# Kernel tuning notes

Hardware: AMD Instinct MI355X
Metric: run time of the kernel (lower is better)

Reference implementation:

```python
import jax, jax.numpy as jnp
import numpy as np

NH, HD, MB = 32, 64, 16        # heads, head_dim, TTT mini-batch size
BASE_LR = 1.0
ROPE_THETA = 10000.0


def _ln(x, w, b, eps):
    mu = x.mean(-1, keepdims=True)
    var = ((x - mu) ** 2).mean(-1, keepdims=True)
    return (x - mu) / jnp.sqrt(var + eps) * w + b


def _rotate_half(x):
    x1, x2 = jnp.split(x, 2, axis=-1)
    return jnp.concatenate([-x2, x1], axis=-1)


def _ln_l2_bwd(x, target, g, b, eps=1e-6):
    # grad of ||LN(x)*g+b - target||^2 / 2 wrt x (fused, as in ttt-lm)
    D = x.shape[-1]
    mu = x.mean(-1, keepdims=True)
    var = ((x - mu) ** 2).mean(-1, keepdims=True)
    std = jnp.sqrt(var + eps)
    xh = (x - mu) / std
    gxh = (g * xh + b - target) * g
    return (D * gxh - gxh.sum(-1, keepdims=True) - xh * (gxh * xh).sum(-1, keepdims=True)) / (D * std)


def _ttt_forward(x, q_w, k_w, v_w, o_w, ttt_lr_w, ttt_lr_b, token_idx_off,
                 ttt_norm_w, ttt_norm_b, W1, b1, post_w, post_b):
    B, L, C = x.shape
    NM = L // MB
    XQ = (x @ q_w).reshape(B, L, NH, HD).transpose(0, 2, 1, 3)  # [B,NH,L,HD]
    XK = (x @ k_w).reshape(B, L, NH, HD).transpose(0, 2, 1, 3)
    XV = (x @ v_w).reshape(B, L, NH, HD).transpose(0, 2, 1, 3)
    # rotary embedding at position_ids % mini_batch_size
    pos = (jnp.arange(L) % MB).astype(jnp.float32)
    inv = 1.0 / (ROPE_THETA ** (jnp.arange(0, HD, 2, dtype=jnp.float32) / HD))
    fr = pos[:, None] * inv[None, :]
    emb = jnp.concatenate([fr, fr], axis=-1)           # [L,HD]
    cos, sin = jnp.cos(emb), jnp.sin(emb)
    XQ = XQ * cos + _rotate_half(XQ) * sin
    XK = XK * cos + _rotate_half(XK) * sin
    # learning-rate gate (eta)
    Xm = x.reshape(B, NM, MB, C)
    ttt_lr = jax.nn.sigmoid(jnp.einsum('bnkc,hdc->bhnkd', Xm, ttt_lr_w)
                            + ttt_lr_b.reshape(1, NH, 1, 1, 1))       # [B,NH,NM,MB,1]
    ttt_lr_eta = BASE_LR * ttt_lr.transpose(0, 1, 2, 4, 3) / HD       # [B,NH,NM,1,MB]
    tok = jnp.maximum(1.0 / jnp.arange(1, MB + 1, dtype=jnp.float32) + token_idx_off, 0.0)
    eta = tok.reshape(1, 1, 1, MB, 1) * ttt_lr_eta                    # [B,NH,NM,MB,MB]

    def tomb(t):  # [B,NH,L,HD] -> [NM,B,NH,MB,HD]
        return t.reshape(B, NH, NM, MB, HD).transpose(2, 0, 1, 3, 4)

    xs = (tomb(XQ), tomb(XK), tomb(XV), eta.transpose(2, 0, 1, 3, 4))
    lw = ttt_norm_w.reshape(1, NH, 1, HD)
    lb = ttt_norm_b.reshape(1, NH, 1, HD)
    tril = jnp.tril(jnp.ones((MB, MB), x.dtype))
    W1s = jnp.broadcast_to(W1, (B, NH, HD, HD)).astype(x.dtype)
    b1s = jnp.broadcast_to(b1, (B, NH, 1, HD)).astype(x.dtype)

    def step(carry, xs_t):
        W1c, b1c = carry
        xq, xk, xv, et = xs_t                      # [B,NH,MB,HD], et [B,NH,MB,MB]
        Z1 = xk @ W1c + b1c
        grad = _ln_l2_bwd(Z1, xv - xk, lw, lb)     # grad of per-head TTT loss wrt Z1
        Attn1 = jnp.tril(xq @ xk.transpose(0, 1, 3, 2))
        b1_bar = b1c - (et * tril) @ grad
        Z1_bar = xq @ W1c - (et * Attn1) @ grad + b1_bar
        last_eta = et[:, :, -1, :, None]           # [B,NH,MB,1]
        W1n = W1c - jnp.einsum('bhki,bhkj->bhij', last_eta * xk, grad)
        b1n = b1c - (last_eta * grad).sum(-2, keepdims=True)
        out = xq + _ln(Z1_bar, lw, lb, 1e-6)
        return (W1n, b1n), out

    _, outs = jax.lax.scan(step, (W1s, b1s), xs)   # outs: [NM,B,NH,MB,HD]
    y = outs.transpose(1, 0, 3, 2, 4).reshape(B, L, C)
    y = _ln(y, post_w, post_b, 1e-6)
    return y @ o_w


def setup_inputs() -> dict:
    key = jax.random.key(0)
    ks = jax.random.split(key, 16)
    B, L, C, DH = 4, 2048, 2048, 1024
    s = 0.02
    return {
        'enc_input': jax.random.normal(ks[0], (B, L, C), jnp.float32),
        'ln1_w': jnp.ones((C,), jnp.float32), 'ln1_b': jnp.zeros((C,), jnp.float32),
        'q_w': jax.random.normal(ks[1], (C, C), jnp.float32) * s,
        'k_w': jax.random.normal(ks[2], (C, C), jnp.float32) * s,
        'v_w': jax.random.normal(ks[3], (C, C), jnp.float32) * s,
        'o_w': jax.random.normal(ks[4], (C, C), jnp.float32) * s,
        'ttt_lr_w': jax.random.normal(ks[5], (NH, 1, C), jnp.float32) * s,
        'ttt_lr_b': jax.random.normal(ks[6], (NH,), jnp.float32) * s,
        'token_idx_off': jax.random.normal(ks[7], (MB,), jnp.float32) * 0.01,
        'ttt_norm_w': jnp.ones((NH, HD), jnp.float32),
        'ttt_norm_b': jnp.zeros((NH, HD), jnp.float32),
        'W1': jax.random.normal(ks[8], (NH, HD, HD), jnp.float32) * s,
        'b1': jnp.zeros((NH, 1, HD), jnp.float32),
        'post_w': jnp.ones((C,), jnp.float32), 'post_b': jnp.zeros((C,), jnp.float32),
        'ffn_ln_w': jnp.ones((C,), jnp.float32), 'ffn_ln_b': jnp.zeros((C,), jnp.float32),
        'w1f': jax.random.normal(ks[9], (C, DH), jnp.float32) * s,
        'b1f': jnp.zeros((DH,), jnp.float32),
        'w2f': jax.random.normal(ks[10], (DH, C), jnp.float32) * s,
        'b2f': jnp.zeros((C,), jnp.float32),
    }


def reference(enc_input, ln1_w, ln1_b, q_w, k_w, v_w, o_w, ttt_lr_w, ttt_lr_b,
              token_idx_off, ttt_norm_w, ttt_norm_b, W1, b1, post_w, post_b,
              ffn_ln_w, ffn_ln_b, w1f, b1f, w2f, b2f):
    # pre-LN (torch default eps=1e-5) + TTT linear block + residual
    x = _ln(enc_input, ln1_w, ln1_b, 1e-5)
    y = _ttt_forward(x, q_w, k_w, v_w, o_w, ttt_lr_w, ttt_lr_b, token_idx_off,
                     ttt_norm_w, ttt_norm_b, W1, b1, post_w, post_b)
    y = y + enc_input
    # position-wise FFN (pre-LN eps=1e-6) + residual; dropout = eval no-op
    z = _ln(y, ffn_ln_w, ffn_ln_b, 1e-6)
    z = jax.nn.relu(z @ w1f + b1f) @ w2f + b2f
    return z + y
```

## Files before the change

### kernel.cpp

```cpp
#include <hip/hip_runtime.h>

typedef unsigned short u16;
typedef __attribute__((ext_vector_type(8))) short short8;
typedef __attribute__((ext_vector_type(8))) unsigned short ushort8;
typedef __attribute__((ext_vector_type(4))) unsigned short us4;
typedef __attribute__((ext_vector_type(4))) float f32x4;
typedef __attribute__((ext_vector_type(2))) float f32x2;
typedef __attribute__((ext_vector_type(2))) unsigned int uint2v;

#define DEV __device__ __forceinline__

DEV float bf2f(u16 u){ union{unsigned int i; float f;} v; v.i = ((unsigned int)u)<<16u; return v.f; }
DEV u16 f2bf(float f){ union{float f; unsigned int i;} v; v.f=f; unsigned int r = v.i + 0x7FFFu + ((v.i>>16)&1u); return (u16)(r>>16); }

DEV void gload16(const u16* g, u16* l){
  __builtin_amdgcn_global_load_lds((const __attribute__((address_space(1))) void*)g,
                                   (__attribute__((address_space(3))) void*)l, 16, 0, 0);
}

DEV float wsum(float v){
  v += __shfl_xor(v, 32, 64);
  v += __shfl_xor(v, 16, 64);
  v += __shfl_xor(v, 8, 64);
  v += __shfl_xor(v, 4, 64);
// ... 92 lines not shown
    for(int r=0;r<4;r++) o[r] = f2bf((a[j][r]-mu)*rstd*wj[r] + bj[r]);
    *(us4*)(outb + (size_t)row*2048 + j*256 + lane*4) = o;
  }
}

__global__ __launch_bounds__(256) void transpose_cast3(
    const float* __restrict__ s0, u16* __restrict__ d0v, int K0, int N0,
    const float* __restrict__ s1, u16* __restrict__ d1v, int K1, int N1,
    const float* __restrict__ s2, u16* __restrict__ d2v, int K2, int N2)
{
  const int z = blockIdx.z;
  const float* src = (z==0)? s0 : (z==1)? s1 : s2;
  u16* dst = (z==0)? d0v : (z==1)? d1v : d2v;
  const int K = (z==0)? K0 : (z==1)? K1 : K2;
  const int N = (z==0)? N0 : (z==1)? N1 : N2;
  const int kb = blockIdx.x*32, nb = blockIdx.y*32;
  if (kb >= K || nb >= N) return;
  __shared__ float tile[32][33];
  const int tx = threadIdx.x & 31, ty = threadIdx.x >> 5;
  #pragma unroll
  for(int i=0;i<4;i++){
    int k = ty + i*8;
    tile[k][tx] = src[(size_t)(kb+k)*N + nb + tx];
  }
  __syncthreads();
  #pragma unroll
  for(int i=0;i<4;i++){
    int nn = ty + i*8;
    dst[(size_t)(nb+nn)*K + kb + tx] = f2bf(tile[tx][nn]);
  }
}

__global__ __launch_bounds__(256) void cast_lrw(const float* __restrict__ lrw, u16* __restrict__ dst)
{
  int i = blockIdx.x*256 + threadIdx.x;
  if (i < 32*2048) dst[i] = f2bf(lrw[i]);
  else dst[i] = 0;
}

__global__ void rope_init(const float* __restrict__ tio, float* __restrict__ cosb,
                          float* __restrict__ sinb, float* __restrict__ tokb)
{
  int t = blockIdx.x*256 + threadIdx.x;
  if (t < 1024){
    int p = t>>6, d = t&63;
    float inv = powf(10000.f, -(float)(2*(d&31))/64.f);
    float fr = (float)p * inv;
    cosb[t] = cosf(fr);
    sinb[t] = sinf(fr);
  }
  if (blockIdx.x==0 && threadIdx.x<16)
    tokb[threadIdx.x] = fmaxf(1.f/(float)(threadIdx.x+1) + tio[threadIdx.x], 0.f);
}

#define MM(MI,NI,AA,BB) acc[MI][NI] = __builtin_amdgcn_mfma_f32_16x16x32_bf16(AA, BB, acc[MI][NI], 0, 0, 0)

#define RD_A(D,KH,MF) (*(const short8*)(ldsb + ((D)<<16) + ((KH)<<14) + (wm<<13) + ((MF)<<10) + loff))
#define RD_B(D,KH,NF) (*(const short8*)(ldsb + ((D)<<16) + 32768 + ((KH)<<14) + (wn<<12) + ((NF)<<10) + loff))

#define PHASE(D,KH,MH,RB,STG,VM) { \
  __builtin_amdgcn_sched_barrier(0); \
  if (RB){ b0 = RD_B(D,KH,0); b1 = RD_B(D,KH,1); b2 = RD_B(D,KH,2); b3 = RD_B(D,KH,3); } \
  short8 a0 = RD_A(D,KH,4*(MH)+0); \
  short8 a1 = RD_A(D,KH,4*(MH)+1); \
  short8 a2 = RD_A(D,KH,4*(MH)+2); \
  short8 a3 = RD_A(D,KH,4*(MH)+3); \
  STG; \
  __builtin_amdgcn_sched_barrier(0); \
  __builtin_amdgcn_s_barrier(); \
  asm volatile("s_waitcnt lgkmcnt(0)" ::: "memory"); \
  __builtin_amdgcn_sched_barrier(0); \
  __builtin_amdgcn_s_setprio(1); \
  MM(4*(MH)+0,0,a0,b0); MM(4*(MH)+1,0,a1,b0); MM(4*(MH)+2,0,a2,b0); MM(4*(MH)+3,0,a3,b0); \
  MM(4*(MH)+0,1,a0,b1); MM(4*(MH)+1,1,a1,b1); MM(4*(MH)+2,1,a2,b1); MM(4*(MH)+3,1,a3,b1); \
  MM(4*(MH)+0,2,a0,b2); MM(4*(MH)+1,2,a1,b2); MM(4*(MH)+2,2,a2,b2); MM(4*(MH)+3,2,a3,b2); \
  MM(4*(MH)+0,3,a0,b3); MM(4*(MH)+1,3,a1,b3); MM(4*(MH)+2,3,a2,b3); MM(4*(MH)+3,3,a3,b3); \
  __builtin_amdgcn_s_setprio(0); \
  if (VM){ asm volatile("s_waitcnt vmcnt(8)" ::: "memory"); } \
  __builtin_amdgcn_sched_barrier(0); \
  __builtin_amdgcn_s_barrier(); \
}

template<int EPI>
__global__ __launch_bounds__(512, 2) void gemm256(
    const u16* __restrict__ A, const u16* __restrict__ Bt,
    float* __restrict__ C, u16* __restrict__ Cb,
    const float* __restrict__ bias, const float* __restrict__ resid,
    const u16* __restrict__ residb,
    int Nld, int Nreal, int K, int ntN)
{
  extern __shared__ u16 lds[];
  const int t = threadIdx.x, lane = t&63, wv = t>>6;
  const int wm = wv>>2, wn = wv&3;
  const int fr = lane&15, kq = lane>>4;

  int bid = blockIdx.x;
  {
    int nwg = gridDim.x;
    int q = nwg>>3, r = nwg&7;
    int x = bid&7, l = bid>>3;
    bid = (x<r) ? (x*(q+1)+l) : (r*(q+1)+(x-r)*q+l);
  }
  const int bm = bid/ntN, bn = bid%ntN;

  f32x4 acc[8][4];
  #pragma unroll
  for(int i=0;i<8;i++)
    #pragma unroll
    for(int j=0;j<4;j++) acc[i][j]=(f32x4){0.f,0.f,0.f,0.f};

  const u16* gA = A  + (size_t)(bm*256)*K;
  const u16* gB = Bt + (size_t)(bn*256)*K;

  const int Ls   = (t&7) ^ ((t>>3)&7);
  const int rstg = ((t>>3)<<1) | (Ls>>2);
  const int cstg = (Ls&3)<<3;
  u16* const ldsw = lds + (wv<<9);

  const int Plane = (((fr&1)<<2) | kq) ^ (fr>>1);
  const int loff  = ((fr>>1)<<7) | (Plane<<4);
  const char* const ldsb = (const char*)lds;

  auto stA = [&](int d, int kh, int kts){
    u16* lb = ldsw + (d<<15) + (kh<<13);
    const u16* g = gA + (size_t)rstg*K + kts + (kh<<5) + cstg;
    gload16(g, lb);
    gload16(g + ((size_t)K<<7), lb + 4096);
  };
  auto stB = [&](int d, int kh, int kts){
    u16* lb = ldsw + (d<<15) + 16384 + (kh<<13);
    const u16* g = gB + (size_t)rstg*K + kts + (kh<<5) + cstg;
    gload16(g, lb);
    gload16(g + ((size_t)K<<7), lb + 4096);
  };

  stA(0,0,0); stB(0,0,0); stA(0,1,0); stB(0,1,0); stA(1,0,64); stB(1,0,64);
  asm volatile("s_waitcnt vmcnt(8)" ::: "memory");
  __builtin_amdgcn_sched_barrier(0);
  __builtin_amdgcn_s_barrier();

  for (int kt = 0; kt < K; kt += 128){
    const int ktp = (kt+128 < K) ? kt+128 : 0;
    const int ktq = (kt+192 < K) ? kt+192 : kt+192-K;
    short8 b0={0},b1={0},b2={0},b3={0};
    PHASE(0,0,0,1, stA(1,1,kt+64), 0)
    PHASE(0,0,1,0, stB(1,1,kt+64), 1)
    PHASE(0,1,0,1, stA(0,0,ktp),   0)
    PHASE(0,1,1,0, stB(0,0,ktp),   1)
    PHASE(1,0,0,1, stA(0,1,ktp),   0)
    PHASE(1,0,1,0, stB(0,1,ktp),   1)
    PHASE(1,1,0,1, stA(1,0,ktq),   0)
    PHASE(1,1,1,0, stB(1,0,ktq),   1)
  }

  const int cr = (lane>>4)<<2, cc = lane&15;
  #pragma unroll
  for(int mi=0;mi<8;mi++){
    #pragma unroll
    for(int ni=0;ni<4;ni++){
      const int row0 = bm*256 + wm*128 + mi*16 + cr;
      const int col  = bn*256 + wn*64  + ni*16 + cc;
      if (col < Nreal){
        #pragma unroll
        for(int rr=0;rr<4;rr++){
          size_t idx = (size_t)(row0+rr)*Nld + col;
          float v = acc[mi][ni][rr];
          if (EPI==1) { v += resid[idx]; Cb[idx] = f2bf(v); }
          else if (EPI==2){ v += bias[col]; v = fmaxf(v, 0.f); Cb[idx] = f2bf(v); }
          else if (EPI==3){ v += bias[col]; v += bf2f(residb[idx]); C[idx] = v; }
          else { Cb[idx] = f2bf(v); }
        }
      }
    }
  }
}

#define W1LD 72
#define XLD  72
#define GTLD 40
#define EKLD 40
#define EALD 40
#define TD2  68

__global__ __launch_bounds__(512, 1) void ttt_scan(
    const u16* __restrict__ XQKV,
    const float* __restrict__ ropec, const float* __restrict__ ropes,
    const float* __restrict__ tokp,
    const float* __restrict__ nw, const float* __restrict__ nb,
    const float* __restrict__ lrb,
    const float* __restrict__ W1i,
    const float* __restrict__ b1i,
    u16* __restrict__ Y)
{
  const int blk = blockIdx.x, b = blk>>5, h = blk&31;
  const int t = threadIdx.x, lane = t&63, wv = t>>6;
  const int fr = lane&15, quad = lane>>4;
  const bool isStager = (wv>=4);
  const int sm = wv-4;

  __shared__ u16 W1bf[2][64*W1LD];
  __shared__ u16 xqbf[3][16*XLD];
  __shared__ u16 xkbf[3][16*XLD];
  __shared__ u16 exkT[3][64*EKLD];
  __shared__ u16 gradTbf[2][64*GTLD];
  __shared__ u16 etaA[2][16*EALD];
  __shared__ float tgT2[3][16*TD2];
  __shared__ float xqT2[3][16*TD2];
  __shared__ float b1s[64];
  __shared__ float lrs[3][16];

  const float lrbh = lrb[h];
  const float ct = tokp[15]*(1.f/64.f);
  const float sg = (lane<32)? -1.f : 1.f;

  f32x2 lwr[16];
  #pragma unroll
  for(int m=0;m<4;m++)
    #pragma unroll
    for(int r=0;r<4;r++){
      int d = m*16+quad*4+r;
      lwr[m*4+r] = (f32x2){nw[h*64+d], nb[h*64+d]};
    }
  float tki[4];
  #pragma unroll
  for(int r=0;r<4;r++) tki[r] = tokp[quad*4+r];

  float ccj[4], ssj[4];
  f32x4 wf0, wf1, wf2, wf3;
  u16 Pq[4], Pk[4], Pv[4], Pl[4];
  if (isStager){
    #pragma unroll
    for(int j=0;j<4;j++){
      ccj[j] = ropec[(sm*4+j)*64 + lane];
      ssj[j] = ropes[(sm*4+j)*64 + lane];
    }
    const float* wsrc = W1i + (size_t)h*4096;
    #pragma unroll
    for(int r=0;r<4;r++){
      int d = sm*16+quad*4+r;
      wf0[r] = wsrc[( 0+fr)*64 + d];
      wf1[r] = wsrc[(16+fr)*64 + d];
      wf2[r] = wsrc[(32+fr)*64 + d];
      wf3[r] = wsrc[(48+fr)*64 + d];
    }
    #pragma unroll
    for(int r=0;r<4;r++){
      int d = sm*16+quad*4+r;
      W1bf[0][d*W1LD +  0 + fr] = f2bf(wf0[r]);
      W1bf[0][d*W1LD + 16 + fr] = f2bf(wf1[r]);
      W1bf[0][d*W1LD + 32 + fr] = f2bf(wf2[r]);
      W1bf[0][d*W1LD + 48 + fr] = f2bf(wf3[r]);
    }
  }
  for(int i=t;i<64*24;i+=512){
    int rr=i/24, cp=16+i%24;
    gradTbf[0][rr*GTLD+cp]=0; gradTbf[1][rr*GTLD+cp]=0;
    exkT[0][rr*EKLD+cp]=0; exkT[1][rr*EKLD+cp]=0; exkT[2][rr*EKLD+cp]=0;
  }
  for(int i=t;i<16*24;i+=512){
    int rr=i/24, cp=16+i%24;
    etaA[0][rr*EALD+cp]=0; etaA[1][rr*EALD+cp]=0;
  }
  if (t<64) b1s[t]=b1i[h*64+t];

  auto loadP = [&](int n){
    const size_t rb = (size_t)b*2048 + n*16;
    #pragma unroll
    for(int j=0;j<4;j++){
      const u16* p = XQKV + (rb+sm*4+j)*6272 + h*64 + lane;
      Pq[j]=p[0]; Pk[j]=p[2048]; Pv[j]=p[4096];
      Pl[j]=XQKV[(rb+sm*4+j)*6272 + 6144 + h];
    }
  };
  auto stage4 = [&](int slot){
    #pragma unroll
    for(int j=0;j<4;j++){
      const int i = sm*4+j;
      float q=bf2f(Pq[j]), k=bf2f(Pk[j]), v=bf2f(Pv[j]);
      float qr = q*ccj[j] + sg*swap32(q)*ssj[j];
      float kr = k*ccj[j] + sg*swap32(k)*ssj[j];
      float lr = 1.f/(1.f + expf(-(bf2f(Pl[j]) + lrbh)));
      xqbf[slot][i*XLD+lane] = f2bf(qr);
      xkbf[slot][i*XLD+lane] = f2bf(kr);
      exkT[slot][lane*EKLD+i] = f2bf(-ct*lr*kr);
      tgT2[slot][i*TD2+lane] = v - kr;
      xqT2[slot][i*TD2+lane] = qr;
      if (lane==0) lrs[slot][i]=lr;
    }
  };

  if (isStager){
    loadP(0);
    stage4(0);
    loadP(1);
  }
  __syncthreads();

  const f32x4 fzero = (f32x4){0.f,0.f,0.f,0.f};

  f32x4 zqP0=fzero, zqP1=fzero, zqP2=fzero, zqP3=fzero;
  f32x4 b1qP0=fzero, b1qP1=fzero, b1qP2=fzero, b1qP3=fzero;

  auto do_out = [&](int p2, int p3, size_t rb){
    short8 be = *(const short8*)&etaA[p2][fr*EALD + quad*8];
    f32x4 c20,c21,c22,c23;
    c20 = __builtin_amdgcn_mfma_f32_16x16x32_bf16(*(const short8*)&gradTbf[p2][( 0+fr)*GTLD + quad*8], be, fzero, 0,0,0);
    c21 = __builtin_amdgcn_mfma_f32_16x16x32_bf16(*(const short8*)&gradTbf[p2][(16+fr)*GTLD + quad*8], be, fzero, 0,0,0);
    c22 = __builtin_amdgcn_mfma_f32_16x16x32_bf16(*(const short8*)&gradTbf[p2][(32+fr)*GTLD + quad*8], be, fzero, 0,0,0);
    c23 = __builtin_amdgcn_mfma_f32_16x16x32_bf16(*(const short8*)&gradTbf[p2][(48+fr)*GTLD + quad*8], be, fzero, 0,0,0);
    f32x4 xqv0 = *(const f32x4*)&xqT2[p3][fr*TD2 +  0 + quad*4];
    f32x4 xqv1 = *(const f32x4*)&xqT2[p3][fr*TD2 + 16 + quad*4];
    f32x4 xqv2 = *(const f32x4*)&xqT2[p3][fr*TD2 + 32 + quad*4];
    f32x4 xqv3 = *(const f32x4*)&xqT2[p3][fr*TD2 + 48 + quad*4];
    f32x4 zb0,zb1,zb2,zb3;
    float s1=0.f, s2=0.f;
    #pragma unroll
    for(int r=0;r<4;r++){
      zb0[r] = zqP0[r] + b1qP0[r] + c20[r];
      zb1[r] = zqP1[r] + b1qP1[r] + c21[r];
      zb2[r] = zqP2[r] + b1qP2[r] + c22[r];
      zb3[r] = zqP3[r] + b1qP3[r] + c23[r];
      s1 += zb0[r]+zb1[r]+zb2[r]+zb3[r];
      s2 += zb0[r]*zb0[r]+zb1[r]*zb1[r]+zb2[r]*zb2[r]+zb3[r]*zb3[r];
    }
    s1 = qsum(s1); s2 = qsum(s2);
    float mu = s1*(1.f/64.f);
    float var = s2*(1.f/64.f) - mu*mu;
    float rstd = rsqrtf(var + 1e-6f);
    #pragma unroll
    for(int m=0;m<4;m++){
      f32x4* zp = (m==0)?&zb0:(m==1)?&zb1:(m==2)?&zb2:&zb3;
      const f32x4* xp = (m==0)?&xqv0:(m==1)?&xqv1:(m==2)?&xqv2:&xqv3;
      us4 o;
      #pragma unroll
      for(int r=0;r<4;r++){
        f32x2 wb = lwr[m*4+r];
        float xh = ((*zp)[r] - mu)*rstd;
        o[r] = f2bf((*xp)[r] + xh*wb[0] + wb[1]);
      }
      *(us4*)&Y[(rb+fr)*2048 + h*64 + m*16 + quad*4] = o;
    }
  };

  int c3 = 0;
  for(int n=0;n<128;n++){
    const int cur2 = n&1, pb2 = cur2^1;
    const int cur3 = c3;
    const int nxt3 = (c3==2)? 0 : c3+1;
    const int pb3  = (c3==0)? 2 : c3-1;
    const size_t rbase = (size_t)b*2048 + n*16;

    if (wv < 2){
      f32x4 b1v0 = *(const f32x4*)&b1s[ 0+quad*4];
      f32x4 b1v1 = *(const f32x4*)&b1s[16+quad*4];
      f32x4 b1v2 = *(const f32x4*)&b1s[32+quad*4];
      f32x4 b1v3 = *(const f32x4*)&b1s[48+quad*4];
      f32x4 tgv0 = *(const f32x4*)&tgT2[cur3][fr*TD2 +  0 + quad*4];
      f32x4 tgv1 = *(const f32x4*)&tgT2[cur3][fr*TD2 + 16 + quad*4];
      f32x4 tgv2 = *(const f32x4*)&tgT2[cur3][fr*TD2 + 32 + quad*4];
      f32x4 tgv3 = *(const f32x4*)&tgT2[cur3][fr*TD2 + 48 + quad*4];
      short8 bk0 = *(const short8*)&xkbf[cur3][fr*XLD + quad*8];
      short8 bk1 = *(const short8*)&xkbf[cur3][fr*XLD + 32 + quad*8];
      f32x4 z0,z1,z2,z3;
      z0 = __builtin_amdgcn_mfma_f32_16x16x32_bf16(*(const short8*)&W1bf[cur2][( 0+fr)*W1LD + quad*8],      bk0, fzero, 0,0,0);
      z0 = __builtin_amdgcn_mfma_f32_16x16x32_bf16(*(const short8*)&W1bf[cur2][( 0+fr)*W1LD + 32 + quad*8], bk1, z0,    0,0,0);
      z1 = __builtin_amdgcn_mfma_f32_16x16x32_bf16(*(const short8*)&W1bf[cur2][(16+fr)*W1LD + quad*8],      bk0, fzero, 0,0,0);
      z1 = __builtin_amdgcn_mfma_f32_16x16x32_bf16(*(const short8*)&W1bf[cur2][(16+fr)*W1LD + 32 + quad*8], bk1, z1,    0,0,0);
      z2 = __builtin_amdgcn_mfma_f32_16x16x32_bf16(*(const short8*)&W1bf[cur2][(32+fr)*W1LD + quad*8],      bk0, fzero, 0,0,0);
      z2 = __builtin_amdgcn_mfma_f32_16x16x32_bf16(*(const short8*)&W1bf[cur2][(32+fr)*W1LD + 32 + quad*8], bk1, z2,    0,0,0);
      z3 = __builtin_amdgcn_mfma_f32_16x16x32_bf16(*(const short8*)&W1bf[cur2][(48+fr)*W1LD + quad*8],      bk0, fzero, 0,0,0);
      z3 = __builtin_amdgcn_mfma_f32_16x16x32_bf16(*(const short8*)&W1bf[cur2][(48+fr)*W1LD + 32 + quad*8], bk1, z3,    0,0,0);
      f32x4 xh0,xh1,xh2,xh3;
      {
        float s1=0.f, s2=0.f;
        #pragma unroll
        for(int r=0;r<4;r++){
          z0[r] += b1v0[r];
          z1[r] += b1v1[r];
          z2[r] += b1v2[r];
          z3[r] += b1v3[r];
          s1 += z0[r]+z1[r]+z2[r]+z3[r];
          s2 += z0[r]*z0[r]+z1[r]*z1[r]+z2[r]*z2[r]+z3[r]*z3[r];
        }
        s1 = qsum(s1); s2 = qsum(s2);
        float mu = s1*(1.f/64.f);
        float var = s2*(1.f/64.f) - mu*mu;
        float rstd = rsqrtf(var + 1e-6f);
        float u1=0.f, u2=0.f;
        #pragma unroll
        for(int m=0;m<4;m++){
          f32x4* zp = (m==0)?&z0:(m==1)?&z1:(m==2)?&z2:&z3;
          f32x4* xp = (m==0)?&xh0:(m==1)?&xh1:(m==2)?&xh2:&xh3;
          const f32x4* tp = (m==0)?&tgv0:(m==1)?&tgv1:(m==2)?&tgv2:&tgv3;
          #pragma unroll
          for(int r=0;r<4;r++){
            f32x2 wb = lwr[m*4+r];
            float xh = ((*zp)[r] - mu)*rstd;
            float gx = (wb[0]*xh + wb[1] - (*tp)[r])*wb[0];
            (*xp)[r] = xh;
            (*zp)[r] = gx;
            u1 += gx; u2 += gx*xh;
          }
        }
        u1 = qsum(u1); u2 = qsum(u2);
        const float c64 = rstd*(1.f/64.f);
        #pragma unroll
        for(int m=0;m<4;m++){
          f32x4* zp = (m==0)?&z0:(m==1)?&z1:(m==2)?&z2:&z3;
          f32x4* xp = (m==0)?&xh0:(m==1)?&xh1:(m==2)?&xh2:&xh3;
          #pragma unroll
          for(int r=0;r<4;r++)
            (*zp)[r] = (64.f*(*zp)[r] - u1 - (*xp)[r]*u2)*c64;
        }
      }
      f32x4 zA = (wv==0)? z0 : z2;
      f32x4 zB = (wv==0)? z1 : z3;
      const int rb0 = wv*32;
      #pragma unroll
      for(int r=0;r<4;r++){
        gradTbf[cur2][(rb0+quad*4+r)*GTLD + fr]    = f2bf(zA[r]);
        gradTbf[cur2][(rb0+16+quad*4+r)*GTLD + fr] = f2bf(zB[r]);
      }
    }
    else if (wv == 2){
      short8 bq0 = *(const short8*)&xqbf[cur3][fr*XLD + quad*8];
      short8 bq1 = *(const short8*)&xqbf[cur3][fr*XLD + 32 + quad*8];
      f32x4 zqN0,zqN1,zqN2,zqN3;
      zqN0 = __builtin_amdgcn_mfma_f32_16x16x32_bf16(*(const short8*)&W1bf[cur2][( 0+fr)*W1LD + quad*8],      bq0, fzero, 0,0,0);
      zqN0 = __builtin_amdgcn_mfma_f32_16x16x32_bf16(*(const short8*)&W1bf[cur2][( 0+fr)*W1LD + 32 + quad*8], bq1, zqN0,  0,0,0);
      zqN1 = __builtin_amdgcn_mfma_f32_16x16x32_bf16(*(const short8*)&W1bf[cur2][(16+fr)*W1LD + quad*8],      bq0, fzero, 0,0,0);
      zqN1 = __builtin_amdgcn_mfma_f32_16x16x32_bf16(*(const short8*)&W1bf[cur2][(16+fr)*W1LD + 32 + quad*8], bq1, zqN1,  0,0,0);
      zqN2 = __builtin_amdgcn_mfma_f32_16x16x32_bf16(*(const short8*)&W1bf[cur2][(32+fr)*W1LD + quad*8],      bq0, fzero, 0,0,0);
      zqN2 = __builtin_amdgcn_mfma_f32_16x16x32_bf16(*(const short8*)&W1bf[cur2][(32+fr)*W1LD + 32 + quad*8], bq1, zqN2,  0,0,0);
      zqN3 = __builtin_amdgcn_mfma_f32_16x16x32_bf16(*(const short8*)&W1bf[cur2][(48+fr)*W1LD + quad*8],      bq0, fzero, 0,0,0);
      zqN3 = __builtin_amdgcn_mfma_f32_16x16x32_bf16(*(const short8*)&W1bf[cur2][(48+fr)*W1LD + 32 + quad*8], bq1, zqN3,  0,0,0);
      if (n > 0) do_out(pb2, pb3, rbase - 16);
      zqP0=zqN0; zqP1=zqN1; zqP2=zqN2; zqP3=zqN3;
      b1qP0 = *(const f32x4*)&b1s[ 0+quad*4];
      b1qP1 = *(const f32x4*)&b1s[16+quad*4];
      b1qP2 = *(const f32x4*)&b1s[32+quad*4];
      b1qP3 = *(const f32x4*)&b1s[48+quad*4];
    }
    else if (wv == 3){
      short8 aq0 = *(const short8*)&xqbf[cur3][fr*XLD + quad*8];
      short8 aq1 = *(const short8*)&xqbf[cur3][fr*XLD + 32 + quad*8];
      short8 bk0 = *(const short8*)&xkbf[cur3][fr*XLD + quad*8];
      short8 bk1 = *(const short8*)&xkbf[cur3][fr*XLD + 32 + quad*8];
      f32x4 at;
      at = __builtin_amdgcn_mfma_f32_16x16x32_bf16(aq0, bk0, fzero, 0,0,0);
      at = __builtin_amdgcn_mfma_f32_16x16x32_bf16(aq1, bk1, at,    0,0,0);
      float lrj = lrs[cur3][fr]*(1.f/64.f);
      #pragma unroll
      for(int r=0;r<4;r++){
        int i = quad*4 + r;
        float val = (fr <= i) ? -tki[r]*lrj*(1.f + at[r]) : 0.f;
        etaA[cur2][i*EALD + fr] = f2bf(val);
      }
    }
    else {
      if (n < 127) stage4(nxt3);
      if (n < 126) loadP(n+2);
    }
    BARS();

    if (isStager){
      short8 ga = *(const short8*)&gradTbf[cur2][(sm*16+fr)*GTLD + quad*8];
      short8 e0 = *(const short8*)&exkT[cur3][( 0+fr)*EKLD + quad*8];
      short8 e1 = *(const short8*)&exkT[cur3][(16+fr)*EKLD + quad*8];
      short8 e2 = *(const short8*)&exkT[cur3][(32+fr)*EKLD + quad*8];
      short8 e3 = *(const short8*)&exkT[cur3][(48+fr)*EKLD + quad*8];
      wf0 = __builtin_amdgcn_mfma_f32_16x16x32_bf16(ga, e0, wf0, 0,0,0);
      wf1 = __builtin_amdgcn_mfma_f32_16x16x32_bf16(ga, e1, wf1, 0,0,0);
      wf2 = __builtin_amdgcn_mfma_f32_16x16x32_bf16(ga, e2, wf2, 0,0,0);
      wf3 = __builtin_amdgcn_mfma_f32_16x16x32_bf16(ga, e3, wf3, 0,0,0);
      #pragma unroll
      for(int r=0;r<4;r++){
        int d = sm*16+quad*4+r;
        W1bf[pb2][d*W1LD +  0 + fr] = f2bf(wf0[r]);
        W1bf[pb2][d*W1LD + 16 + fr] = f2bf(wf1[r]);
        W1bf[pb2][d*W1LD + 32 + fr] = f2bf(wf2[r]);
        W1bf[pb2][d*W1LD + 48 + fr] = f2bf(wf3[r]);
      }
    }
    else if (wv == 3){
      const int d = lane;
      short8 g0 = *(const short8*)&gradTbf[cur2][d*GTLD + 0];
      short8 g1 = *(const short8*)&gradTbf[cur2][d*GTLD + 8];
      float s = 0.f;
      #pragma unroll
      for(int j=0;j<8;j++) s += lrs[cur3][j]   * bf2f((u16)g0[j]);
      #pragma unroll
      for(int j=0;j<8;j++) s += lrs[cur3][8+j] * bf2f((u16)g1[j]);
      b1s[d] -= ct * s;
    }
    BARS();
    c3 = nxt3;
  }

  if (wv == 2) do_out(1, 1, (size_t)b*2048 + 127*16);
}

extern "C" void kernel_launch(void* const* d_in, const int* in_sizes, int n_in,
                              void* d_out, int out_size, void* d_ws, size_t ws_size,
                              hipStream_t stream)
{
  const float* enc   = (const float*)d_in[0];
  const float* ln1w  = (const float*)d_in[1];
  const float* ln1b  = (const float*)d_in[2];
  const float* qw    = (const float*)d_in[3];
  const float* kw    = (const float*)d_in[4];
  const float* vw    = (const float*)d_in[5];
  const float* ow    = (const float*)d_in[6];
  const float* lrw   = (const float*)d_in[7];
  const float* lrb   = (const float*)d_in[8];
  const float* tio   = (const float*)d_in[9];
  const float* tnw   = (const float*)d_in[10];
  const float* tnb   = (const float*)d_in[11];
  const float* W1i   = (const float*)d_in[12];
  const float* b1i   = (const float*)d_in[13];
  const float* postw = (const float*)d_in[14];
  const float* postb = (const float*)d_in[15];
  const float* flnw  = (const float*)d_in[16];
  const float* flnb  = (const float*)d_in[17];
  const float* w1f   = (const float*)d_in[18];
  const float* b1f   = (const float*)d_in[19];
  const float* w2f   = (const float*)d_in[20];
  const float* b2f   = (const float*)d_in[21];
  float* out = (float*)d_out;

  char* ws = (char*)d_ws;
  size_t off = 0;
  auto alloc = [&](size_t bytes)->void*{ void* p = ws + off; off += (bytes + 255) & ~(size_t)255; return p; };
  u16*   regA  = (u16*)  alloc(8192ull*2048*2);
  u16*   wqkvT = (u16*)  alloc(6400ull*2048*2);
  u16*   XQKV  = (u16*)  alloc(8192ull*6272*2);
  u16*   ybb   = (u16*)  alloc(8192ull*2048*2);
  u16*   y2b   = (u16*)  alloc(8192ull*2048*2);
  float* ropec = (float*)alloc(1024*4);
  float* ropes = (float*)alloc(1024*4);
  float* tokb  = (float*)alloc(64*4);

  u16* oT   = wqkvT;
  u16* w1fT = wqkvT + 2048ull*2048;
  u16* w2fT = w1fT + 1024ull*2048;
  u16* hbf  = XQKV;

  static bool s_attr = false;
  if (!s_attr){
    s_attr = true;
    (void)hipFuncSetAttribute(reinterpret_cast<const void*>(gemm256<4>), hipFuncAttributeMaxDynamicSharedMemorySize, 131072);
    (void)hipFuncSetAttribute(reinterpret_cast<const void*>(gemm256<1>), hipFuncAttributeMaxDynamicSharedMemorySize, 131072);
    (void)hipFuncSetAttribute(reinterpret_cast<const void*>(gemm256<2>), hipFuncAttributeMaxDynamicSharedMemorySize, 131072);
    (void)hipFuncSetAttribute(reinterpret_cast<const void*>(gemm256<3>), hipFuncAttributeMaxDynamicSharedMemorySize, 131072);
  }

  rope_init<<<4, 256, 0, stream>>>(tio, ropec, ropes, tokb);

  transpose_cast3<<<dim3(64,64,3), 256, 0, stream>>>(
      qw, wqkvT,                2048, 2048,
      kw, wqkvT + 2048ull*2048, 2048, 2048,
      vw, wqkvT + 4096ull*2048, 2048, 2048);
  cast_lrw<<<2048, 256, 0, stream>>>(lrw, wqkvT + 6144ull*2048);

  ln_row<<<2048, 256, 0, stream>>>(enc, ln1w, ln1b, 1e-5f, regA);

  gemm256<4><<<32*25, 512, 131072, stream>>>(regA, wqkvT, nullptr, XQKV,
                                             nullptr, nullptr, nullptr, 6272, 6272, 2048, 25);

  transpose_cast3<<<dim3(64,64,3), 256, 0, stream>>>(
      ow,  oT,   2048, 2048,
      w1f, w1fT, 2048, 1024,
      w2f, w2fT, 1024, 2048);

  ttt_scan<<<128, 512, 0, stream>>>(XQKV, ropec, ropes, tokb, tnw, tnb, lrb, W1i, b1i, ybb);

  ln_rowb<<<2048, 256, 0, stream>>>(ybb, postw, postb, 1e-6f, regA);
  gemm256<1><<<32*8, 512, 131072, stream>>>(regA, oT, nullptr, y2b,
                                            nullptr, enc, nullptr, 2048, 2048, 2048, 8);

  ln_rowb<<<2048, 256, 0, stream>>>(y2b, flnw, flnb, 1e-6f, regA);
  gemm256<2><<<32*4, 512, 131072, stream>>>(regA, w1fT, nullptr, hbf,
                                            b1f, nullptr, nullptr, 1024, 1024, 2048, 4);
  gemm256<3><<<32*8, 512, 131072, stream>>>(hbf, w2fT, out, nullptr,
                                            b2f, nullptr, y2b, 2048, 2048, 1024, 8);
}
```

Measured before the change: 748.1 us.

## Fuse QKV GEMM with TTT scan using per-row-tile completion counters

Merges the QKV projection GEMM and the sequential TTT scan into one persistent kernel. 128 blocks act as pure GEMM workers, and 128 scan blocks each compute one GEMM tile before running their scan. Row-tile completion is published through atomic counters, and the scan waits on these counters before consuming each 256-row chunk, so the scan can start while later tiles are still being produced. The tile order is permuted to finish early rows for all batches first. In exchange it relies on spin-waiting with forward-progress assumptions, moves the scan's shared memory to the dynamic allocation, and raises the scan kernel's occupancy bound to 2.

```diff
diff --git a/kernel.cpp b/kernel.cpp
--- a/kernel.cpp
+++ b/kernel.cpp
@@ -198,26 +198,14 @@
 }
 
 template<int EPI>
-__global__ __launch_bounds__(512, 2) void gemm256(
-    const u16* __restrict__ A, const u16* __restrict__ Bt,
-    float* __restrict__ C, u16* __restrict__ Cb,
-    const float* __restrict__ bias, const float* __restrict__ resid,
-    const u16* __restrict__ residb,
-    int Nld, int Nreal, int K, int ntN)
-{
-  extern __shared__ u16 lds[];
+DEV void gemm_tile(const u16* A, const u16* Bt,
+                   float* C, u16* Cb,
+                   const float* bias, const float* resid, const u16* residb,
+                   int Nld, int Nreal, int K, int bm, int bn, u16* lds)
+{
   const int t = threadIdx.x, lane = t&63, wv = t>>6;
   const int wm = wv>>2, wn = wv&3;
   const int fr = lane&15, kq = lane>>4;
-
-  int bid = blockIdx.x;
-  {
-    int nwg = gridDim.x;
-    int q = nwg>>3, r = nwg&7;
-    int x = bid&7, l = bid>>3;
-    bid = (x<r) ? (x*(q+1)+l) : (r*(q+1)+(x-r)*q+l);
-  }
-  const int bm = bid/ntN, bn = bid%ntN;
 
   f32x4 acc[8][4];
   #pragma unroll
@@ -291,39 +279,102 @@
   }
 }
 
+template<int EPI>
+__global__ __launch_bounds__(512, 2) void gemm256(
+    const u16* __restrict__ A, const u16* __restrict__ Bt,
+    float* __restrict__ C, u16* __restrict__ Cb,
+    const float* __restrict__ bias, const float* __restrict__ resid,
+    const u16* __restrict__ residb,
+    int Nld, int Nreal, int K, int ntN)
+{
+  extern __shared__ u16 lds[];
+  int bid = blockIdx.x;
+  {
+    int nwg = gridDim.x;
+    int q = nwg>>3, r = nwg&7;
+    int x = bid&7, l = bid>>3;
+    bid = (x<r) ? (x*(q+1)+l) : (r*(q+1)+(x-r)*q+l);
+  }
+  gemm_tile<EPI>(A, Bt, C, Cb, bias, resid, residb, Nld, Nreal, K, bid/ntN, bid%ntN, lds);
+}
+
 #define W1LD 72
 #define XLD  72
 #define GTLD 40
 #define EKLD 40
 #define EALD 40
 #define TD2  68
-
-__global__ __launch_bounds__(512, 1) void ttt_scan(
-    const u16* __restrict__ XQKV,
+#define W1SZ 4608
+#define XSZ  1152
+#define EKSZ 2560
+#define GTSZ 2560
+#define EASZ 640
+#define TDSZ 1088
+
+__global__ __launch_bounds__(512, 2) void qkv_scan(
+    const u16* __restrict__ Abf, const u16* __restrict__ Bt, u16* __restrict__ XQKV,
+    int* __restrict__ cnts,
     const float* __restrict__ ropec, const float* __restrict__ ropes,
     const float* __restrict__ tokp,
     const float* __restrict__ nw, const float* __restrict__ nb,
     const float* __restrict__ lrb,
-    const float* __restrict__ W1i,
-    const float* __restrict__ b1i,
+    const float* __restrict__ W1i, const float* __restrict__ b1i,
     u16* __restrict__ Y)
 {
-  const int blk = blockIdx.x, b = blk>>5, h = blk&31;
-  const int t = threadIdx.x, lane = t&63, wv = t>>6;
+  extern __shared__ u16 lds[];
+  const int t = threadIdx.x;
+
+  auto flagtile = [&](int mt){
+    __threadfence();
+    __syncthreads();
+    if (t==0) __hip_atomic_fetch_add(&cnts[mt], 1, __ATOMIC_RELEASE, __HIP_MEMORY_SCOPE_AGENT);
+  };
+
+  if (blockIdx.x < 128){
+    for (int w = blockIdx.x; w < 672; w += 128){
+      int mi = w/25, nt = w - mi*25;
+      int mt = ((mi&3)<<3) + (mi>>2);
+      gemm_tile<4>(Abf, Bt, nullptr, XQKV, nullptr, nullptr, nullptr, 6272, 6272, 2048, mt, nt, lds);
+      flagtile(mt);
+      __syncthreads();
+    }
+    return;
+  }
+
+  {
+    int w = 672 + (blockIdx.x - 128);
+    int mi = w/25, nt = w - mi*25;
+    int mt = ((mi&3)<<3) + (mi>>2);
+    gemm_tile<4>(Abf, Bt, nullptr, XQKV, nullptr, nullptr, nullptr, 6272, 6272, 2048, mt, nt, lds);
+    flagtile(mt);
+    __syncthreads();
+  }
+
+  const int blk = blockIdx.x - 128, b = blk>>5, h = blk&31;
+  const int lane = t&63, wv = t>>6;
   const int fr = lane&15, quad = lane>>4;
   const bool isStager = (wv>=4);
   const int sm = wv-4;
 
-  __shared__ u16 W1bf[2][64*W1LD];
-  __shared__ u16 xqbf[3][16*XLD];
-  __shared__ u16 xkbf[3][16*XLD];
-  __shared__ u16 exkT[3][64*EKLD];
-  __shared__ u16 gradTbf[2][64*GTLD];
-  __shared__ u16 etaA[2][16*EALD];
-  __shared__ float tgT2[3][16*TD2];
-  __shared__ float xqT2[3][16*TD2];
-  __shared__ float b1s[64];
-  __shared__ float lrs[3][16];
+  u16*  const W1bf_ = lds;
+  u16*  const xqbf_ = lds + 9216;
+  u16*  const xkbf_ = lds + 12672;
+  u16*  const exkT_ = lds + 16128;
+  u16*  const gqT_  = lds + 23808;
+  u16*  const etA_  = lds + 28928;
+  float* const tgT_ = (float*)(lds + 30208);
+  float* const xqT_ = tgT_ + 3264;
+  float* const b1s_ = xqT_ + 3264;
+  float* const lrs_ = b1s_ + 64;
+
+  auto waitm = [&](int mt){
+    if (t==0){
+      while (__hip_atomic_load(&cnts[mt], __ATOMIC_ACQUIRE, __HIP_MEMORY_SCOPE_AGENT) < 25)
+        __builtin_amdgcn_s_sleep(8);
+    }
+    __syncthreads();
+    __threadfence();
+  };
 
   const float lrbh = lrb[h];
   const float ct = tokp[15]*(1.f/64.f);
@@ -362,22 +413,22 @@
     #pragma unroll
     for(int r=0;r<4;r++){
       int d = sm*16+quad*4+r;
-      W1bf[0][d*W1LD +  0 + fr] = f2bf(wf0[r]);
-      W1bf[0][d*W1LD + 16 + fr] = f2bf(wf1[r]);
-      W1bf[0][d*W1LD + 32 + fr] = f2bf(wf2[r]);
-      W1bf[0][d*W1LD + 48 + fr] = f2bf(wf3[r]);
+      W1bf_[d*W1LD +  0 + fr] = f2bf(wf0[r]);
+      W1bf_[d*W1LD + 16 + fr] = f2bf(wf1[r]);
+      W1bf_[d*W1LD + 32 + fr] = f2bf(wf2[r]);
+      W1bf_[d*W1LD + 48 + fr] = f2bf(wf3[r]);
     }
   }
   for(int i=t;i<64*24;i+=512){
     int rr=i/24, cp=16+i%24;
-    gradTbf[0][rr*GTLD+cp]=0; gradTbf[1][rr*GTLD+cp]=0;
-    exkT[0][rr*EKLD+cp]=0; exkT[1][rr*EKLD+cp]=0; exkT[2][rr*EKLD+cp]=0;
+    gqT_[rr*GTLD+cp]=0; gqT_[GTSZ + rr*GTLD+cp]=0;
+    exkT_[rr*EKLD+cp]=0; exkT_[EKSZ + rr*EKLD+cp]=0; exkT_[2*EKSZ + rr*EKLD+cp]=0;
   }
   for(int i=t;i<16*24;i+=512){
     int rr=i/24, cp=16+i%24;
-    etaA[0][rr*EALD+cp]=0; etaA[1][rr*EALD+cp]=0;
-  }
-  if (t<64) b1s[t]=b1i[h*64+t];
+    etA_[rr*EALD+cp]=0; etA_[EASZ + rr*EALD+cp]=0;
+  }
+  if (t<64) b1s_[t]=b1i[h*64+t];
 
   auto loadP = [&](int n){
     const size_t rb = (size_t)b*2048 + n*16;
@@ -396,15 +447,16 @@
       float qr = q*ccj[j] + sg*swap32(q)*ssj[j];
       float kr = k*ccj[j] + sg*swap32(k)*ssj[j];
       float lr = 1.f/(1.f + expf(-(bf2f(Pl[j]) + lrbh)));
-      xqbf[slot][i*XLD+lane] = f2bf(qr);
-      xkbf[slot][i*XLD+lane] = f2bf(kr);
-      exkT[slot][lane*EKLD+i] = f2bf(-ct*lr*kr);
-      tgT2[slot][i*TD2+lane] = v - kr;
-      xqT2[slot][i*TD2+lane] = qr;
-      if (lane==0) lrs[slot][i]=lr;
+      xqbf_[slot*XSZ + i*XLD+lane] = f2bf(qr);
+      xkbf_[slot*XSZ + i*XLD+lane] = f2bf(kr);
+      exkT_[slot*EKSZ + lane*EKLD+i] = f2bf(-ct*lr*kr);
+      tgT_[slot*TDSZ + i*TD2+lane] = v - kr;
+      xqT_[slot*TDSZ + i*TD2+lane] = qr;
+      if (lane==0) lrs_[slot*16+i]=lr;
     }
   };
 
+  waitm(b*8);
   if (isStager){
     loadP(0);
     stage4(0);
@@ -418,16 +470,16 @@
   f32x4 b1qP0=fzero, b1qP1=fzero, b1qP2=fzero, b1qP3=fzero;
 
   auto do_out = [&](int p2, int p3, size_t rb){
-    short8 be = *(const short8*)&etaA[p2][fr*EALD + quad*8];
+    short8 be = *(const short8*)&etA_[p2*EASZ + fr*EALD + quad*8];
     f32x4 c20,c21,c22,c23;
-    c20 = __builtin_amdgcn_mfma_f32_16x16x32_bf16(*(const short8*)&gradTbf[p2][( 0+fr)*GTLD + quad*8], be, fzero, 0,0,0);
-    c21 = __builtin_amdgcn_mfma_f32_16x16x32_bf16(*(const short8*)&gradTbf[p2][(16+fr)*GTLD + quad*8], be, fzero, 0,0,0);
-    c22 = __builtin_amdgcn_mfma_f32_16x16x32_bf16(*(const short8*)&gradTbf[p2][(32+fr)*GTLD + quad*8], be, fzero, 0,0,0);
-    c23 = __builtin_amdgcn_mfma_f32_16x16x32_bf16(*(const short8*)&gradTbf[p2][(48+fr)*GTLD + quad*8], be, fzero, 0,0,0);
-    f32x4 xqv0 = *(const f32x4*)&xqT2[p3][fr*TD2 +  0 + quad*4];
-    f32x4 xqv1 = *(const f32x4*)&xqT2[p3][fr*TD2 + 16 + quad*4];
-    f32x4 xqv2 = *(const f32x4*)&xqT2[p3][fr*TD2 + 32 + quad*4];
-    f32x4 xqv3 = *(const f32x4*)&xqT2[p3][fr*TD2 + 48 + quad*4];
+    c20 = __builtin_amdgcn_mfma_f32_16x16x32_bf16(*(const short8*)&gqT_[p2*GTSZ + ( 0+fr)*GTLD + quad*8], be, fzero, 0,0,0);
+    c21 = __builtin_amdgcn_mfma_f32_16x16x32_bf16(*(const short8*)&gqT_[p2*GTSZ + (16+fr)*GTLD + quad*8], be, fzero, 0,0,0);
+    c22 = __builtin_amdgcn_mfma_f32_16x16x32_bf16(*(const short8*)&gqT_[p2*GTSZ + (32+fr)*GTLD + quad*8], be, fzero, 0,0,0);
+    c23 = __builtin_amdgcn_mfma_f32_16x16x32_bf16(*(const short8*)&gqT_[p2*GTSZ + (48+fr)*GTLD + quad*8], be, fzero, 0,0,0);
+    f32x4 xqv0 = *(const f32x4*)&xqT_[p3*TDSZ + fr*TD2 +  0 + quad*4];
+    f32x4 xqv1 = *(const f32x4*)&xqT_[p3*TDSZ + fr*TD2 + 16 + quad*4];
+    f32x4 xqv2 = *(const f32x4*)&xqT_[p3*TDSZ + fr*TD2 + 32 + quad*4];
+    f32x4 xqv3 = *(const f32x4*)&xqT_[p3*TDSZ + fr*TD2 + 48 + quad*4];
     f32x4 zb0,zb1,zb2,zb3;
     float s1=0.f, s2=0.f;
     #pragma unroll
@@ -466,26 +518,28 @@
     const int pb3  = (c3==0)? 2 : c3-1;
     const size_t rbase = (size_t)b*2048 + n*16;
 
+    if (n < 126 && ((n+2)&15)==0) waitm(b*8 + ((n+2)>>4));
+
     if (wv < 2){
-      f32x4 b1v0 = *(const f32x4*)&b1s[ 0+quad*4];
-      f32x4 b1v1 = *(const f32x4*)&b1s[16+quad*4];
-      f32x4 b1v2 = *(const f32x4*)&b1s[32+quad*4];
-      f32x4 b1v3 = *(const f32x4*)&b1s[48+quad*4];
-      f32x4 tgv0 = *(const f32x4*)&tgT2[cur3][fr*TD2 +  0 + quad*4];
-      f32x4 tgv1 = *(const f32x4*)&tgT2[cur3][fr*TD2 + 16 + quad*4];
-      f32x4 tgv2 = *(const f32x4*)&tgT2[cur3][fr*TD2 + 32 + quad*4];
-      f32x4 tgv3 = *(const f32x4*)&tgT2[cur3][fr*TD2 + 48 + quad*4];
-      short8 bk0 = *(const short8*)&xkbf[cur3][fr*XLD + quad*8];
-      short8 bk1 = *(const short8*)&xkbf[cur3][fr*XLD + 32 + quad*8];
+      f32x4 b1v0 = *(const f32x4*)&b1s_[ 0+quad*4];
+      f32x4 b1v1 = *(const f32x4*)&b1s_[16+quad*4];
+      f32x4 b1v2 = *(const f32x4*)&b1s_[32+quad*4];
+      f32x4 b1v3 = *(const f32x4*)&b1s_[48+quad*4];
+      f32x4 tgv0 = *(const f32x4*)&tgT_[cur3*TDSZ + fr*TD2 +  0 + quad*4];
+      f32x4 tgv1 = *(const f32x4*)&tgT_[cur3*TDSZ + fr*TD2 + 16 + quad*4];
+      f32x4 tgv2 = *(const f32x4*)&tgT_[cur3*TDSZ + fr*TD2 + 32 + quad*4];
+      f32x4 tgv3 = *(const f32x4*)&tgT_[cur3*TDSZ + fr*TD2 + 48 + quad*4];
+      short8 bk0 = *(const short8*)&xkbf_[cur3*XSZ + fr*XLD + quad*8];
+      short8 bk1 = *(const short8*)&xkbf_[cur3*XSZ + fr*XLD + 32 + quad*8];
       f32x4 z0,z1,z2,z3;
-      z0 = __builtin_amdgcn_mfma_f32_16x16x32_bf16(*(const short8*)&W1bf[cur2][( 0+fr)*W1LD + quad*8],      bk0, fzero, 0,0,0);
-      z0 = __builtin_amdgcn_mfma_f32_16x16x32_bf16(*(const short8*)&W1bf[cur2][( 0+fr)*W1LD + 32 + quad*8], bk1, z0,    0,0,0);
-      z1 = __builtin_amdgcn_mfma_f32_16x16x32_bf16(*(const short8*)&W1bf[cur2][(16+fr)*W1LD + quad*8],      bk0, fzero, 0,0,0);
-      z1 = __builtin_amdgcn_mfma_f32_16x16x32_bf16(*(const short8*)&W1bf[cur2][(16+fr)*W1LD + 32 + quad*8], bk1, z1,    0,0,0);
-      z2 = __builtin_amdgcn_mfma_f32_16x16x32_bf16(*(const short8*)&W1bf[cur2][(32+fr)*W1LD + quad*8],      bk0, fzero, 0,0,0);
-      z2 = __builtin_amdgcn_mfma_f32_16x16x32_bf16(*(const short8*)&W1bf[cur2][(32+fr)*W1LD + 32 + quad*8], bk1, z2,    0,0,0);
-      z3 = __builtin_amdgcn_mfma_f32_16x16x32_bf16(*(const short8*)&W1bf[cur2][(48+fr)*W1LD + quad*8],      bk0, fzero, 0,0,0);
-      z3 = __builtin_amdgcn_mfma_f32_16x16x32_bf16(*(const short8*)&W1bf[cur2][(48+fr)*W1LD + 32 + quad*8], bk1, z3,    0,0,0);
+      z0 = __builtin_amdgcn_mfma_f32_16x16x32_bf16(*(const short8*)&W1bf_[cur2*W1SZ + ( 0+fr)*W1LD + quad*8],      bk0, fzero, 0,0,0);
+      z0 = __builtin_amdgcn_mfma_f32_16x16x32_bf16(*(const short8*)&W1bf_[cur2*W1SZ + ( 0+fr)*W1LD + 32 + quad*8], bk1, z0,    0,0,0);
+      z1 = __builtin_amdgcn_mfma_f32_16x16x32_bf16(*(const short8*)&W1bf_[cur2*W1SZ + (16+fr)*W1LD + quad*8],      bk0, fzero, 0,0,0);
+      z1 = __builtin_amdgcn_mfma_f32_16x16x32_bf16(*(const short8*)&W1bf_[cur2*W1SZ + (16+fr)*W1LD + 32 + quad*8], bk1, z1,    0,0,0);
+      z2 = __builtin_amdgcn_mfma_f32_16x16x32_bf16(*(const short8*)&W1bf_[cur2*W1SZ + (32+fr)*W1LD + quad*8],      bk0, fzero, 0,0,0);
+      z2 = __builtin_amdgcn_mfma_f32_16x16x32_bf16(*(const short8*)&W1bf_[cur2*W1SZ + (32+fr)*W1LD + 32 + quad*8], bk1, z2,    0,0,0);
+      z3 = __builtin_amdgcn_mfma_f32_16x16x32_bf16(*(const short8*)&W1bf_[cur2*W1SZ + (48+fr)*W1LD + quad*8],      bk0, fzero, 0,0,0);
+      z3 = __builtin_amdgcn_mfma_f32_16x16x32_bf16(*(const short8*)&W1bf_[cur2*W1SZ + (48+fr)*W1LD + 32 + quad*8], bk1, z3,    0,0,0);
       f32x4 xh0,xh1,xh2,xh3;
       {
         float s1=0.f, s2=0.f;
@@ -534,43 +588,43 @@
       const int rb0 = wv*32;
       #pragma unroll
       for(int r=0;r<4;r++){
-        gradTbf[cur2][(rb0+quad*4+r)*GTLD + fr]    = f2bf(zA[r]);
-        gradTbf[cur2][(rb0+16+quad*4+r)*GTLD + fr] = f2bf(zB[r]);
+        gqT_[cur2*GTSZ + (rb0+quad*4+r)*GTLD + fr]    = f2bf(zA[r]);
+        gqT_[cur2*GTSZ + (rb0+16+quad*4+r)*GTLD + fr] = f2bf(zB[r]);
       }
     }
     else if (wv == 2){
-      short8 bq0 = *(const short8*)&xqbf[cur3][fr*XLD + quad*8];
-      short8 bq1 = *(const short8*)&xqbf[cur3][fr*XLD + 32 + quad*8];
+      short8 bq0 = *(const short8*)&xqbf_[cur3*XSZ + fr*XLD + quad*8];
+      short8 bq1 = *(const short8*)&xqbf_[cur3*XSZ + fr*XLD + 32 + quad*8];
       f32x4 zqN0,zqN1,zqN2,zqN3;
-      zqN0 = __builtin_amdgcn_mfma_f32_16x16x32_bf16(*(const short8*)&W1bf[cur2][( 0+fr)*W1LD + quad*8],      bq0, fzero, 0,0,0);
-      zqN0 = __builtin_amdgcn_mfma_f32_16x16x32_bf16(*(const short8*)&W1bf[cur2][( 0+fr)*W1LD + 32 + quad*8], bq1, zqN0,  0,0,0);
-      zqN1 = __builtin_amdgcn_mfma_f32_16x16x32_bf16(*(const short8*)&W1bf[cur2][(16+fr)*W1LD + quad*8],      bq0, fzero, 0,0,0);
-      zqN1 = __builtin_amdgcn_mfma_f32_16x16x32_bf16(*(const short8*)&W1bf[cur2][(16+fr)*W1LD + 32 + quad*8], bq1, zqN1,  0,0,0);
-      zqN2 = __builtin_amdgcn_mfma_f32_16x16x32_bf16(*(const short8*)&W1bf[cur2][(32+fr)*W1LD + quad*8],      bq0, fzero, 0,0,0);
-      zqN2 = __builtin_amdgcn_mfma_f32_16x16x32_bf16(*(const short8*)&W1bf[cur2][(32+fr)*W1LD + 32 + quad*8], bq1, zqN2,  0,0,0);
-      zqN3 = __builtin_amdgcn_mfma_f32_16x16x32_bf16(*(const short8*)&W1bf[cur2][(48+fr)*W1LD + quad*8],      bq0, fzero, 0,0,0);
-      zqN3 = __builtin_amdgcn_mfma_f32_16x16x32_bf16(*(const short8*)&W1bf[cur2][(48+fr)*W1LD + 32 + quad*8], bq1, zqN3,  0,0,0);
+      zqN0 = __builtin_amdgcn_mfma_f32_16x16x32_bf16(*(const short8*)&W1bf_[cur2*W1SZ + ( 0+fr)*W1LD + quad*8],      bq0, fzero, 0,0,0);
+      zqN0 = __builtin_amdgcn_mfma_f32_16x16x32_bf16(*(const short8*)&W1bf_[cur2*W1SZ + ( 0+fr)*W1LD + 32 + quad*8], bq1, zqN0,  0,0,0);
+      zqN1 = __builtin_amdgcn_mfma_f32_16x16x32_bf16(*(const short8*)&W1bf_[cur2*W1SZ + (16+fr)*W1LD + quad*8],      bq0, fzero, 0,0,0);
+      zqN1 = __builtin_amdgcn_mfma_f32_16x16x32_bf16(*(const short8*)&W1bf_[cur2*W1SZ + (16+fr)*W1LD + 32 + quad*8], bq1, zqN1,  0,0,0);
+      zqN2 = __builtin_amdgcn_mfma_f32_16x16x32_bf16(*(const short8*)&W1bf_[cur2*W1SZ + (32+fr)*W1LD + quad*8],      bq0, fzero, 0,0,0);
+      zqN2 = __builtin_amdgcn_mfma_f32_16x16x32_bf16(*(const short8*)&W1bf_[cur2*W1SZ + (32+fr)*W1LD + 32 + quad*8], bq1, zqN2,  0,0,0);
+      zqN3 = __builtin_amdgcn_mfma_f32_16x16x32_bf16(*(const short8*)&W1bf_[cur2*W1SZ + (48+fr)*W1LD + quad*8],      bq0, fzero, 0,0,0);
+      zqN3 = __builtin_amdgcn_mfma_f32_16x16x32_bf16(*(const short8*)&W1bf_[cur2*W1SZ + (48+fr)*W1LD + 32 + quad*8], bq1, zqN3,  0,0,0);
       if (n > 0) do_out(pb2, pb3, rbase - 16);
       zqP0=zqN0; zqP1=zqN1; zqP2=zqN2; zqP3=zqN3;
-      b1qP0 = *(const f32x4*)&b1s[ 0+quad*4];
-      b1qP1 = *(const f32x4*)&b1s[16+quad*4];
-      b1qP2 = *(const f32x4*)&b1s[32+quad*4];
-      b1qP3 = *(const f32x4*)&b1s[48+quad*4];
+      b1qP0 = *(const f32x4*)&b1s_[ 0+quad*4];
+      b1qP1 = *(const f32x4*)&b1s_[16+quad*4];
+      b1qP2 = *(const f32x4*)&b1s_[32+quad*4];
+      b1qP3 = *(const f32x4*)&b1s_[48+quad*4];
     }
     else if (wv == 3){
-      short8 aq0 = *(const short8*)&xqbf[cur3][fr*XLD + quad*8];
-      short8 aq1 = *(const short8*)&xqbf[cur3][fr*XLD + 32 + quad*8];
-      short8 bk0 = *(const short8*)&xkbf[cur3][fr*XLD + quad*8];
-      short8 bk1 = *(const short8*)&xkbf[cur3][fr*XLD + 32 + quad*8];
+      short8 aq0 = *(const short8*)&xqbf_[cur3*XSZ + fr*XLD + quad*8];
+      short8 aq1 = *(const short8*)&xqbf_[cur3*XSZ + fr*XLD + 32 + quad*8];
+      short8 bk0 = *(const short8*)&xkbf_[cur3*XSZ + fr*XLD + quad*8];
+      short8 bk1 = *(const short8*)&xkbf_[cur3*XSZ + fr*XLD + 32 + quad*8];
       f32x4 at;
       at = __builtin_amdgcn_mfma_f32_16x16x32_bf16(aq0, bk0, fzero, 0,0,0);
       at = __builtin_amdgcn_mfma_f32_16x16x32_bf16(aq1, bk1, at,    0,0,0);
-      float lrj = lrs[cur3][fr]*(1.f/64.f);
+      float lrj = lrs_[cur3*16+fr]*(1.f/64.f);
       #pragma unroll
       for(int r=0;r<4;r++){
         int i = quad*4 + r;
         float val = (fr <= i) ? -tki[r]*lrj*(1.f + at[r]) : 0.f;
-        etaA[cur2][i*EALD + fr] = f2bf(val);
+        etA_[cur2*EASZ + i*EALD + fr] = f2bf(val);
       }
     }
     else {
@@ -580,11 +634,11 @@
     BARS();
 
     if (isStager){
-      short8 ga = *(const short8*)&gradTbf[cur2][(sm*16+fr)*GTLD + quad*8];
-      short8 e0 = *(const short8*)&exkT[cur3][( 0+fr)*EKLD + quad*8];
-      short8 e1 = *(const short8*)&exkT[cur3][(16+fr)*EKLD + quad*8];
-      short8 e2 = *(const short8*)&exkT[cur3][(32+fr)*EKLD + quad*8];
-      short8 e3 = *(const short8*)&exkT[cur3][(48+fr)*EKLD + quad*8];
+      short8 ga = *(const short8*)&gqT_[cur2*GTSZ + (sm*16+fr)*GTLD + quad*8];
+      short8 e0 = *(const short8*)&exkT_[cur3*EKSZ + ( 0+fr)*EKLD + quad*8];
+      short8 e1 = *(const short8*)&exkT_[cur3*EKSZ + (16+fr)*EKLD + quad*8];
+      short8 e2 = *(const short8*)&exkT_[cur3*EKSZ + (32+fr)*EKLD + quad*8];
+      short8 e3 = *(const short8*)&exkT_[cur3*EKSZ + (48+fr)*EKLD + quad*8];
       wf0 = __builtin_amdgcn_mfma_f32_16x16x32_bf16(ga, e0, wf0, 0,0,0);
       wf1 = __builtin_amdgcn_mfma_f32_16x16x32_bf16(ga, e1, wf1, 0,0,0);
       wf2 = __builtin_amdgcn_mfma_f32_16x16x32_bf16(ga, e2, wf2, 0,0,0);
@@ -592,22 +646,22 @@
       #pragma unroll
       for(int r=0;r<4;r++){
         int d = sm*16+quad*4+r;
-        W1bf[pb2][d*W1LD +  0 + fr] = f2bf(wf0[r]);
-        W1bf[pb2][d*W1LD + 16 + fr] = f2bf(wf1[r]);
-        W1bf[pb2][d*W1LD + 32 + fr] = f2bf(wf2[r]);
-        W1bf[pb2][d*W1LD + 48 + fr] = f2bf(wf3[r]);
+        W1bf_[pb2*W1SZ + d*W1LD +  0 + fr] = f2bf(wf0[r]);
+        W1bf_[pb2*W1SZ + d*W1LD + 16 + fr] = f2bf(wf1[r]);
+        W1bf_[pb2*W1SZ + d*W1LD + 32 + fr] = f2bf(wf2[r]);
+        W1bf_[pb2*W1SZ + d*W1LD + 48 + fr] = f2bf(wf3[r]);
       }
     }
     else if (wv == 3){
       const int d = lane;
-      short8 g0 = *(const short8*)&gradTbf[cur2][d*GTLD + 0];
-      short8 g1 = *(const short8*)&gradTbf[cur2][d*GTLD + 8];
+      short8 g0 = *(const short8*)&gqT_[cur2*GTSZ + d*GTLD + 0];
+      short8 g1 = *(const short8*)&gqT_[cur2*GTSZ + d*GTLD + 8];
       float s = 0.f;
       #pragma unroll
-      for(int j=0;j<8;j++) s += lrs[cur3][j]   * bf2f((u16)g0[j]);
+      for(int j=0;j<8;j++) s += lrs_[cur3*16+j]   * bf2f((u16)g0[j]);
       #pragma unroll
-      for(int j=0;j<8;j++) s += lrs[cur3][8+j] * bf2f((u16)g1[j]);
-      b1s[d] -= ct * s;
+      for(int j=0;j<8;j++) s += lrs_[cur3*16+8+j] * bf2f((u16)g1[j]);
+      b1s_[d] -= ct * s;
     }
     BARS();
     c3 = nxt3;
@@ -655,6 +709,7 @@
   float* ropec = (float*)alloc(1024*4);
   float* ropes = (float*)alloc(1024*4);
   float* tokb  = (float*)alloc(64*4);
+  int*   cnts  = (int*)  alloc(128);
 
   u16* oT   = wqkvT;
   u16* w1fT = wqkvT + 2048ull*2048;
@@ -664,7 +719,7 @@
   static bool s_attr = false;
   if (!s_attr){
     s_attr = true;
-    (void)hipFuncSetAttribute(reinterpret_cast<const void*>(gemm256<4>), hipFuncAttributeMaxDynamicSharedMemorySize, 131072);
+    (void)hipFuncSetAttribute(reinterpret_cast<const void*>(qkv_scan),  hipFuncAttributeMaxDynamicSharedMemorySize, 131072);
     (void)hipFuncSetAttribute(reinterpret_cast<const void*>(gemm256<1>), hipFuncAttributeMaxDynamicSharedMemorySize, 131072);
     (void)hipFuncSetAttribute(reinterpret_cast<const void*>(gemm256<2>), hipFuncAttributeMaxDynamicSharedMemorySize, 131072);
     (void)hipFuncSetAttribute(reinterpret_cast<const void*>(gemm256<3>), hipFuncAttributeMaxDynamicSharedMemorySize, 131072);
@@ -680,15 +735,14 @@
 
   ln_row<<<2048, 256, 0, stream>>>(enc, ln1w, ln1b, 1e-5f, regA);
 
-  gemm256<4><<<32*25, 512, 131072, stream>>>(regA, wqkvT, nullptr, XQKV,
-                                             nullptr, nullptr, nullptr, 6272, 6272, 2048, 25);
+  (void)hipMemsetAsync(cnts, 0, 128, stream);
+  qkv_scan<<<256, 512, 131072, stream>>>(regA, wqkvT, XQKV, cnts,
+                                         ropec, ropes, tokb, tnw, tnb, lrb, W1i, b1i, ybb);
 
   transpose_cast3<<<dim3(64,64,3), 256, 0, stream>>>(
       ow,  oT,   2048, 2048,
       w1f, w1fT, 2048, 1024,
       w2f, w2fT, 1024, 2048);
-
-  ttt_scan<<<128, 512, 0, stream>>>(XQKV, ropec, ropes, tokb, tnw, tnb, lrb, W1i, b1i, ybb);
 
   ln_rowb<<<2048, 256, 0, stream>>>(ybb, postw, postb, 1e-6f, regA);
   gemm256<1><<<32*8, 512, 131072, stream>>>(regA, oT, nullptr, y2b,
```

New measurement: 1.570 ms. 110% more time.
